# Kernel optimization log

Hardware: AMD Instinct MI355X
Metric: run time of the kernel (lower is better)

Reference implementation:

```python
import jax, jax.numpy as jnp
import numpy as np

N_NODES = 100000

def graph_conv(x, src, dst, W_rel, W_root, b, num_nodes):
    # PyG GraphConv: out_i = lin_rel(sum_{j in N(i)} x_j) + lin_root(x_i)
    agg = jax.ops.segment_sum(x[src], dst, num_segments=num_nodes)  # [N, F_in]
    return agg @ W_rel + x @ W_root + b


def setup_inputs() -> dict:
    key = jax.random.key(0)
    ks = jax.random.split(key, 8)
    z = jax.random.normal(ks[0], (N_NODES, 64), dtype=jnp.float32)
    edge_index = jax.random.randint(ks[1], (2, 1600000), 0, N_NODES, dtype=jnp.int64)
    def glorot(k, fi, fo):
        s = (6.0 / (fi + fo)) ** 0.5
        return jax.random.uniform(k, (fi, fo), dtype=jnp.float32, minval=-s, maxval=s)
    return {
        "z": z,
        "edge_index": edge_index,
        "W_rel1": glorot(ks[2], 64, 32), "W_root1": glorot(ks[3], 64, 32), "b1": jnp.zeros((32,), jnp.float32),
        "W_rel2": glorot(ks[4], 32, 16), "W_root2": glorot(ks[5], 32, 16), "b2": jnp.zeros((16,), jnp.float32),
        "W_rel3": glorot(ks[6], 16, 2), "W_root3": glorot(ks[7], 16, 2), "b3": jnp.zeros((2,), jnp.float32),
    }


def reference(z, edge_index, W_rel1, W_root1, b1, W_rel2, W_root2, b2, W_rel3, W_root3, b3):
    src, dst = edge_index[0], edge_index[1]
    h = graph_conv(z, src, dst, W_rel1, W_root1, b1, N_NODES)
    h = jax.nn.relu(h)
    h = graph_conv(h, src, dst, W_rel2, W_root2, b2, N_NODES)
    h = jax.nn.relu(h)
    h = graph_conv(h, src, dst, W_rel3, W_root3, b3, N_NODES)
    return jax.nn.softmax(h, axis=-1)
```

## Files before the change

kernel.cpp:

```cpp
#include <hip/hip_runtime.h>


#define RNODES 128
#define NB_MAX 1024
#define CH 4096
#define CMAX 512

template <int Fin, int Fout, bool RELU>
__global__ void linear_q2_kernel(const float* __restrict__ x,
                                 const float* __restrict__ Wrel,
                                 const float* __restrict__ Wroot,
                                 const float* __restrict__ bias,
                                 short* __restrict__ t,
                                 float* __restrict__ tscale,
                                 float* __restrict__ acc, int N) {
    const bool rootTask = (blockIdx.y != 0);
    const float* __restrict__ W = rootTask ? Wroot : Wrel;

    int n = blockIdx.x * blockDim.x + threadIdx.x;
    if (n >= N) return;

    float o[Fout];
#pragma unroll
    for (int f = 0; f < Fout; ++f) o[f] = 0.f;

    const float* xr = x + (size_t)n * Fin;
#pragma unroll
    for (int k = 0; k < Fin; k += 4) {
        float4 v = *(const float4*)(xr + k);
        if (RELU) {
            v.x = fmaxf(v.x, 0.f); v.y = fmaxf(v.y, 0.f);
            v.z = fmaxf(v.z, 0.f); v.w = fmaxf(v.w, 0.f);
        }
        const float xv[4] = {v.x, v.y, v.z, v.w};
#pragma unroll
        for (int kk = 0; kk < 4; ++kk) {
            const float* wr = W + (size_t)(k + kk) * Fout;
#pragma unroll
            for (int f = 0; f < Fout; ++f)
                o[f] = fmaf(xv[kk], wr[f], o[f]);
        }
    }

    if (rootTask) {
#pragma unroll
        for (int f = 0; f < Fout; ++f) o[f] += bias[f];
        float* arow = acc + (size_t)n * Fout;
        if constexpr (Fout >= 4) {
#pragma unroll
            for (int f = 0; f < Fout; f += 4)
                *(float4*)(arow + f) = make_float4(o[f], o[f+1], o[f+2], o[f+3]);
        } else {
            *(float2*)arow = make_float2(o[0], o[1]);
        }
    } else {
        float m = 0.f;
#pragma unroll
        for (int f = 0; f < Fout; ++f) m = fmaxf(m, fabsf(o[f]));
        const float inv = (m > 0.f) ? (32767.0f / m) : 0.f;
        const float sc  = m * (1.0f / 32767.0f);

        short q[Fout];
#pragma unroll
        for (int f = 0; f < Fout; ++f) q[f] = (short)__float2int_rn(o[f] * inv);

        if constexpr (Fout == 32) {
            tscale[n] = sc;
            short* trow = t + (size_t)n * 32;
#pragma unroll
            for (int f = 0; f < 32; f += 8)
                *(int4*)(trow + f) = *(const int4*)(q + f);
        } else if constexpr (Fout == 16) {
            short* trow = t + (size_t)n * 32;
            *(int4*)(trow)     = *(const int4*)(q);
            *(int4*)(trow + 8) = *(const int4*)(q + 8);
            ((float*)trow)[8]  = sc;
        } else {
            int2 r;
            r.x = (int)(unsigned short)q[0] | ((int)q[1] << 16);
            r.y = __float_as_int(sc);
            *(int2*)(t + (size_t)n * 4) = r;
        }
    }
}

template <int Fin, int Fout, bool RELU>
__global__ void linear2_kernel(const float* __restrict__ x,
                               const float* __restrict__ Wrel,
                               const float* __restrict__ Wroot,
                               const float* __restrict__ bias,
                               float* __restrict__ t,
                               float* __restrict__ acc, int N) {
    const bool rootTask = (blockIdx.y != 0);
    const float* __restrict__ W = rootTask ? Wroot : Wrel;
    float* __restrict__ outp    = rootTask ? acc : t;

    int n = blockIdx.x * blockDim.x + threadIdx.x;
    if (n >= N) return;

    float o[Fout];
#pragma unroll
    for (int f = 0; f < Fout; ++f) o[f] = 0.f;

    const float* xr = x + (size_t)n * Fin;
#pragma unroll
    for (int k = 0; k < Fin; k += 4) {
        float4 v = *(const float4*)(xr + k);
        if (RELU) {
            v.x = fmaxf(v.x, 0.f); v.y = fmaxf(v.y, 0.f);
            v.z = fmaxf(v.z, 0.f); v.w = fmaxf(v.w, 0.f);
        }
        const float xv[4] = {v.x, v.y, v.z, v.w};
#pragma unroll
        for (int kk = 0; kk < 4; ++kk) {
            const float* wr = W + (size_t)(k + kk) * Fout;
#pragma unroll
            for (int f = 0; f < Fout; ++f)
                o[f] = fmaf(xv[kk], wr[f], o[f]);
        }
    }
    if (rootTask) {
#pragma unroll
        for (int f = 0; f < Fout; ++f) o[f] += bias[f];
    }
    float* op = outp + (size_t)n * Fout;
    if constexpr (Fout >= 4) {
#pragma unroll
        for (int f = 0; f < Fout; f += 4)
            *(float4*)(op + f) = make_float4(o[f], o[f + 1], o[f + 2], o[f + 3]);
    } else {
        *(float2*)op = make_float2(o[0], o[1]);
    }
}

__global__ void hist_chunked_kernel(const int* __restrict__ dst,
                                    int* __restrict__ chunkhist,
                                    int nE, int NB) {
    __shared__ int h[NB_MAX];
    const int c  = blockIdx.x;
    const int e0 = c * CH, e1 = min(e0 + CH, nE);
    for (int b = threadIdx.x; b < NB; b += blockDim.x) h[b] = 0;
    __syncthreads();
    for (int e = e0 + threadIdx.x; e < e1; e += blockDim.x)
        atomicAdd(&h[dst[e] >> 7], 1);
    __syncthreads();
    for (int b = threadIdx.x; b < NB; b += blockDim.x)
        chunkhist[(size_t)c * NB + b] = h[b];
}

__global__ void scan_chunkhist_kernel(int* __restrict__ chunkhist,
                                      int* __restrict__ gtotal,
                                      int C, int NB) {
    __shared__ int s[CMAX];
    const int b = blockIdx.x;
    const int t = threadIdx.x;
    int v = (t < C) ? chunkhist[(size_t)t * NB + b] : 0;
    s[t] = v;
    __syncthreads();
    for (int off = 1; off < CMAX; off <<= 1) {
        int u = (t >= off) ? s[t - off] : 0;
        __syncthreads();
        s[t] += u;
        __syncthreads();
    }
    if (t < C) chunkhist[(size_t)t * NB + b] = s[t] - v;
    if (t == CMAX - 1) gtotal[b] = s[t];
}

__global__ void scan_buckets_kernel(const int* __restrict__ gtotal,
                                    int* __restrict__ bptr, int NB, int nE) {
    __shared__ int s[NB_MAX];
    int t = threadIdx.x;
    int own = (t < NB) ? gtotal[t] : 0;
    s[t] = own;
    __syncthreads();
    for (int off = 1; off < NB_MAX; off <<= 1) {
        int v = (t >= off) ? s[t - off] : 0;
        __syncthreads();
        s[t] += v;
        __syncthreads();
    }
    if (t < NB) bptr[t] = s[t] - own;
    if (t == 0) bptr[NB] = nE;
}

__global__ void bucketize_det_kernel(const int* __restrict__ src,
                                     const int* __restrict__ dst,
                                     const int* __restrict__ chunkpre,
                                     const int* __restrict__ bptr,
                                     unsigned int* __restrict__ records,
                                     int nE, int NB) {
    __shared__ int lcur[NB_MAX];
    const int c  = blockIdx.x;
    const int e0 = c * CH, e1 = min(e0 + CH, nE);
    for (int b = threadIdx.x; b < NB; b += blockDim.x)
        lcur[b] = bptr[b] + chunkpre[(size_t)c * NB + b];
    __syncthreads();
    for (int e = e0 + threadIdx.x; e < e1; e += blockDim.x) {
        int d = dst[e];
        int b = d >> 7;
        int pos = atomicAdd(&lcur[b], 1);
        records[pos] = (unsigned int)src[e] | ((unsigned int)(d & 127) << 17);
    }
}

__global__ void place_merge_kernel(const unsigned int* __restrict__ records,
                                   const int* __restrict__ bptr,
                                   int* __restrict__ rowptr,
                                   int* __restrict__ srcs_sorted,
                                   int N, int nE, int NB) {
    __shared__ int hist[RNODES];
    __shared__ int s[RNODES];
    __shared__ int lcur[RNODES];
    const int b    = blockIdx.x;
    const int base = b * RNODES;
    const int nn   = min(RNODES, N - base);
    const int beg  = bptr[b], end = bptr[b + 1];
    const int t    = threadIdx.x;

    if (t < RNODES) hist[t] = 0;
    __syncthreads();
    for (int i = beg + t; i < end; i += blockDim.x)
        atomicAdd(&hist[records[i] >> 17], 1);
    __syncthreads();

    if (t < RNODES) s[t] = hist[t];
    __syncthreads();
    for (int off = 1; off < RNODES; off <<= 1) {
        int v = (t < RNODES && t >= off) ? s[t - off] : 0;
        __syncthreads();
        if (t < RNODES && t >= off) s[t] += v;
        __syncthreads();
    }
    if (t < nn) {
        int ex = beg + s[t] - hist[t];
        rowptr[base + t] = ex;
        lcur[t] = ex;
    }
    if (b == NB - 1 && t == 0) rowptr[N] = nE;
    __syncthreads();

    for (int i = beg + t; i < end; i += blockDim.x) {
        unsigned int rec = records[i];
        int pos = atomicAdd(&lcur[rec >> 17], 1);
        srcs_sorted[pos] = (int)(rec & 0x1FFFFu);
    }
}

template <int F, bool SOFTMAX>
__global__ void gather_agg_q_kernel(const short* __restrict__ t,
                                    const float* __restrict__ tscale,
                                    const int* __restrict__ rowptr,
                                    const int* __restrict__ srcs,
                                    const float* __restrict__ rootacc,
                                    float* __restrict__ out, int N) {
    constexpr int P = (F >= 4) ? (F / 2) : 1;
    constexpr int S = F / 2;
    int tid = blockIdx.x * blockDim.x + threadIdx.x;
    int n  = (P == 1) ? tid : (tid / P);
    int fp = (P == 1) ? 0   : (tid & (P - 1));
    if (n >= N) return;

    const int* tp = (const int*)t;
    int beg = rowptr[n], end = rowptr[n + 1];
    float sx = 0.f, sy = 0.f;
    int e = beg;
    for (; e + 8 <= end; e += 8) {
        int s[8];
#pragma unroll
        for (int u = 0; u < 8; ++u) s[u] = srcs[e + u];
        int q[8]; float sc[8];
#pragma unroll
        for (int u = 0; u < 8; ++u) {
            q[u]  = tp[s[u] * S + fp];
            sc[u] = tscale[s[u]];
        }
#pragma unroll
        for (int u = 0; u < 8; ++u) {
            float lo = (float)((short)(q[u] & 0xFFFF));
            float hi = (float)(q[u] >> 16);
            sx = fmaf(sc[u], lo, sx);
            sy = fmaf(sc[u], hi, sy);
        }
    }
    for (; e < end; ++e) {
        int s0 = srcs[e];
        int qv = tp[s0 * S + fp];
        float sc = tscale[s0];
        sx = fmaf(sc, (float)((short)(qv & 0xFFFF)), sx);
        sy = fmaf(sc, (float)(qv >> 16), sy);
    }

    const float2 r0 = *(const float2*)(rootacc + (size_t)n * F + 2 * fp);
    float a = r0.x + sx, b = r0.y + sy;
    if (!SOFTMAX) {
        *(float2*)(out + (size_t)n * F + 2 * fp) = make_float2(a, b);
    } else {
        float m = fmaxf(a, b);
        float ea = __expf(a - m), eb = __expf(b - m);
        float inv = 1.0f / (ea + eb);
        *(float2*)(out + (size_t)n * 2) = make_float2(ea * inv, eb * inv);
    }
}

__global__ void gather16_inl_kernel(const short* __restrict__ t,
                                    const int* __restrict__ rowptr,
                                    const int* __restrict__ srcs,
                                    const float* __restrict__ rootacc,
                                    float* __restrict__ out, int N) {
    int tid = blockIdx.x * blockDim.x + threadIdx.x;
    int n  = tid >> 3;
    int fp = tid & 7;
    if (n >= N) return;

    const int* tp = (const int*)t;
    int beg = rowptr[n], end = rowptr[n + 1];
    float sx = 0.f, sy = 0.f;
    int e = beg;
    for (; e + 8 <= end; e += 8) {
        int s[8];
#pragma unroll
        for (int u = 0; u < 8; ++u) s[u] = srcs[e + u];
        int q[8]; float sc[8];
#pragma unroll
        for (int u = 0; u < 8; ++u) {
            const int* row = tp + (size_t)s[u] * 16;
            q[u]  = row[fp];
            sc[u] = __int_as_float(row[8]);
        }
#pragma unroll
        for (int u = 0; u < 8; ++u) {
            sx = fmaf(sc[u], (float)((short)(q[u] & 0xFFFF)), sx);
            sy = fmaf(sc[u], (float)(q[u] >> 16), sy);
        }
    }
    for (; e < end; ++e) {
        const int* row = tp + (size_t)srcs[e] * 16;
        int qv = row[fp];
        float sc = __int_as_float(row[8]);
        sx = fmaf(sc, (float)((short)(qv & 0xFFFF)), sx);
        sy = fmaf(sc, (float)(qv >> 16), sy);
    }

    const float2 r0 = *(const float2*)(rootacc + (size_t)n * 16 + 2 * fp);
    *(float2*)(out + (size_t)n * 16 + 2 * fp) = make_float2(r0.x + sx, r0.y + sy);
}

__global__ void gather2_inl_kernel(const short* __restrict__ t,
                                   const int* __restrict__ rowptr,
                                   const int* __restrict__ srcs,
                                   const float* __restrict__ rootacc,
                                   float* __restrict__ out, int N) {
    int tid = blockIdx.x * blockDim.x + threadIdx.x;
    int n  = tid >> 2;
    int fp = tid & 3;
    if (n >= N) return;

    const int2* tp = (const int2*)t;
    int beg = rowptr[n], end = rowptr[n + 1];
    float sx = 0.f, sy = 0.f;
    int e = beg + fp;
    for (; e + 12 < end; e += 16) {
        int s0 = srcs[e], s1 = srcs[e + 4], s2 = srcs[e + 8], s3 = srcs[e + 12];
        int2 r0 = tp[s0], r1 = tp[s1], r2 = tp[s2], r3 = tp[s3];
        sx = fmaf(__int_as_float(r0.y), (float)((short)(r0.x & 0xFFFF)), sx);
        sy = fmaf(__int_as_float(r0.y), (float)(r0.x >> 16), sy);
        sx = fmaf(__int_as_float(r1.y), (float)((short)(r1.x & 0xFFFF)), sx);
        sy = fmaf(__int_as_float(r1.y), (float)(r1.x >> 16), sy);
        sx = fmaf(__int_as_float(r2.y), (float)((short)(r2.x & 0xFFFF)), sx);
        sy = fmaf(__int_as_float(r2.y), (float)(r2.x >> 16), sy);
        sx = fmaf(__int_as_float(r3.y), (float)((short)(r3.x & 0xFFFF)), sx);
        sy = fmaf(__int_as_float(r3.y), (float)(r3.x >> 16), sy);
    }
    for (; e < end; e += 4) {
        int2 r = tp[srcs[e]];
        sx = fmaf(__int_as_float(r.y), (float)((short)(r.x & 0xFFFF)), sx);
        sy = fmaf(__int_as_float(r.y), (float)(r.x >> 16), sy);
    }
    sx += __shfl_xor(sx, 1, 64); sy += __shfl_xor(sy, 1, 64);
    sx += __shfl_xor(sx, 2, 64); sy += __shfl_xor(sy, 2, 64);

    if (fp == 0) {
        const float2 r0 = *(const float2*)(rootacc + (size_t)n * 2);
        float a = r0.x + sx, b = r0.y + sy;
        float m = fmaxf(a, b);
        float ea = __expf(a - m), eb = __expf(b - m);
        float inv = 1.0f / (ea + eb);
        *(float2*)(out + (size_t)n * 2) = make_float2(ea * inv, eb * inv);
    }
}

template <int F>
__global__ void scatter_kernel(const float* __restrict__ t,
                               const int* __restrict__ src,
                               const int* __restrict__ dst,
                               float* __restrict__ acc, int nE) {
    int tid = blockIdx.x * blockDim.x + threadIdx.x;
    int e = tid / F;
    if (e >= nE) return;
    int f = tid & (F - 1);
    atomicAdd(acc + (long)dst[e] * F + f, t[(long)src[e] * F + f]);
}

__global__ void softmax2_kernel(const float* __restrict__ h, float* __restrict__ out, int N) {
    int n = blockIdx.x * blockDim.x + threadIdx.x;
    if (n >= N) return;
    float a = h[2 * n], b = h[2 * n + 1];
    float m = fmaxf(a, b);
    float ea = __expf(a - m), eb = __expf(b - m);
    float inv = 1.0f / (ea + eb);
    out[2 * n] = ea * inv;
    out[2 * n + 1] = eb * inv;
}

extern "C" void kernel_launch(void* const* d_in, const int* in_sizes, int n_in,
                              void* d_out, int out_size, void* d_ws, size_t ws_size,
                              hipStream_t stream) {
    const float* z      = (const float*)d_in[0];
    const int*   ei     = (const int*)d_in[1];
    const float* Wrel1  = (const float*)d_in[2];
    const float* Wroot1 = (const float*)d_in[3];
    const float* b1     = (const float*)d_in[4];
    const float* Wrel2  = (const float*)d_in[5];
    const float* Wroot2 = (const float*)d_in[6];
    const float* b2     = (const float*)d_in[7];
    const float* Wrel3  = (const float*)d_in[8];
    const float* Wroot3 = (const float*)d_in[9];
    const float* b3     = (const float*)d_in[10];

    const int N  = in_sizes[0] / 64;
    const int nE = in_sizes[1] / 2;
    const int* src = ei;
    const int* dst = ei + nE;
    const int NB = (N + RNODES - 1) / RNODES;
    const int C  = (nE + CH - 1) / CH;

    char* wsb = (char*)d_ws;
    size_t off = 0;
    auto take = [&](size_t bytes) -> void* {
        void* p = (void*)(wsb + off);
        off = (off + bytes + 255) & ~(size_t)255;
        return p;
    };
    int*          chunkhist   = (int*)take((size_t)CMAX * NB_MAX * 4);
    int*          gtotal      = (int*)take((size_t)NB_MAX * 4);
    int*          bptr        = (int*)take((size_t)(NB_MAX + 1) * 4);
    unsigned int* records     = (unsigned int*)take((size_t)nE * 4);
    int*          rowptr      = (int*)take((size_t)(N + 1) * 4);
    int*          srcs_sorted = (int*)take((size_t)nE * 4);
    short*        t1          = (short*)take((size_t)N * 32 * 2);
    float*        s1          = (float*)take((size_t)N * 4);
    float*        h1          = (float*)take((size_t)N * 32 * 4);
    short*        t2          = (short*)take((size_t)N * 64);
    float*        h2          = (float*)take((size_t)N * 16 * 4);
    short*        t3          = (short*)take((size_t)N * 8);
    float*        h3          = (float*)take((size_t)N * 2 * 4);
    const size_t needed = off;

    const int B = 256;
    const int nodeBlocks = (N + B - 1) / B;
    const dim3 linGrid(nodeBlocks, 2);
    const bool packOK = (N <= (1 << 17)) && (NB <= NB_MAX) && (C <= CMAX);

    if (ws_size >= needed && packOK) {
        hist_chunked_kernel<<<C, 512, 0, stream>>>(dst, chunkhist, nE, NB);
        scan_chunkhist_kernel<<<NB, CMAX, 0, stream>>>(chunkhist, gtotal, C, NB);
        scan_buckets_kernel<<<1, NB_MAX, 0, stream>>>(gtotal, bptr, NB, nE);
        bucketize_det_kernel<<<C, 512, 0, stream>>>(src, dst, chunkhist, bptr, records, nE, NB);
        place_merge_kernel<<<NB, 512, 0, stream>>>(records, bptr, rowptr, srcs_sorted, N, nE, NB);

        linear_q2_kernel<64, 32, false><<<linGrid, B, 0, stream>>>(
            z, Wrel1, Wroot1, b1, t1, s1, h1, N);
        gather_agg_q_kernel<32, false><<<((size_t)N * 16 + B - 1) / B, B, 0, stream>>>(
            t1, s1, rowptr, srcs_sorted, h1, h1, N);

        linear_q2_kernel<32, 16, true><<<linGrid, B, 0, stream>>>(
            h1, Wrel2, Wroot2, b2, t2, nullptr, h2, N);
        gather16_inl_kernel<<<((size_t)N * 8 + B - 1) / B, B, 0, stream>>>(
            t2, rowptr, srcs_sorted, h2, h2, N);

        linear_q2_kernel<16, 2, true><<<linGrid, B, 0, stream>>>(
            h2, Wrel3, Wroot3, b3, t3, nullptr, h3, N);
        gather2_inl_kernel<<<((size_t)N * 4 + B - 1) / B, B, 0, stream>>>(
            t3, rowptr, srcs_sorted, h3, (float*)d_out, N);
    } else {
        float* regionA = (float*)d_ws;
        float* regionB = regionA + (size_t)N * 32;
        float* ft1 = regionA;
        float* fh1 = regionB;
        float* ft2 = regionA;
        float* fh2 = regionA + (size_t)N * 16;
        float* ft3 = regionB;
        float* fh3 = regionB + (size_t)N * 2;
        linear2_kernel<64, 32, false><<<linGrid, B, 0, stream>>>(z, Wrel1, Wroot1, b1, ft1, fh1, N);
        scatter_kernel<32><<<((size_t)nE * 32 + B - 1) / B, B, 0, stream>>>(ft1, src, dst, fh1, nE);
        linear2_kernel<32, 16, true><<<linGrid, B, 0, stream>>>(fh1, Wrel2, Wroot2, b2, ft2, fh2, N);
        scatter_kernel<16><<<((size_t)nE * 16 + B - 1) / B, B, 0, stream>>>(ft2, src, dst, fh2, nE);
        linear2_kernel<16, 2, true><<<linGrid, B, 0, stream>>>(fh2, Wrel3, Wroot3, b3, ft3, fh3, N);
        scatter_kernel<2><<<((size_t)nE * 2 + B - 1) / B, B, 0, stream>>>(ft3, src, dst, fh3, nE);
        softmax2_kernel<<<nodeBlocks, B, 0, stream>>>(fh3, (float*)d_out, N);
    }
}
```

Measured before the change: 243.0 us.

## Fuse layer-1 linear into sort kernels and drop bucket-scan launch

The layer-1 rel and root linear passes are folded into the histogram and chunk-scan kernels as extra grid rows (blockIdx.y). This lets the dense compute share launches with, and overlap, the latency-bound sort stages. The standalone bucket-scan kernel is removed: bucketize recomputes the bucket prefix in shared memory in every block, and place_merge reduces gtotal per block to find its range. This cuts two launches and one dependency step, at the cost of redundant per-block scans and reductions and larger 1024-thread blocks.

```diff
diff --git a/kernel.cpp b/kernel.cpp
--- a/kernel.cpp
+++ b/kernel.cpp
@@ -5,6 +5,79 @@
 #define NB_MAX 1024
 #define CH 4096
 #define CMAX 512
+
+template <int Fin, int Fout, bool RELU>
+__device__ __forceinline__ void lin_compute(const float* __restrict__ x,
+                                            const float* __restrict__ W,
+                                            int n, float* o) {
+#pragma unroll
+    for (int f = 0; f < Fout; ++f) o[f] = 0.f;
+    const float* xr = x + (size_t)n * Fin;
+#pragma unroll
+    for (int k = 0; k < Fin; k += 4) {
+        float4 v = *(const float4*)(xr + k);
+        if (RELU) {
+            v.x = fmaxf(v.x, 0.f); v.y = fmaxf(v.y, 0.f);
+            v.z = fmaxf(v.z, 0.f); v.w = fmaxf(v.w, 0.f);
+        }
+        const float xv[4] = {v.x, v.y, v.z, v.w};
+#pragma unroll
+        for (int kk = 0; kk < 4; ++kk) {
+            const float* wr = W + (size_t)(k + kk) * Fout;
+#pragma unroll
+            for (int f = 0; f < Fout; ++f)
+                o[f] = fmaf(xv[kk], wr[f], o[f]);
+        }
+    }
+}
+
+template <int Fout>
+__device__ __forceinline__ void store_quant(short* __restrict__ t,
+                                            float* __restrict__ tscale,
+                                            int n, const float* o) {
+    float m = 0.f;
+#pragma unroll
+    for (int f = 0; f < Fout; ++f) m = fmaxf(m, fabsf(o[f]));
+    const float inv = (m > 0.f) ? (32767.0f / m) : 0.f;
+    const float sc  = m * (1.0f / 32767.0f);
+    short q[Fout];
+#pragma unroll
+    for (int f = 0; f < Fout; ++f) q[f] = (short)__float2int_rn(o[f] * inv);
+
+    if constexpr (Fout == 32) {
+        tscale[n] = sc;
+        short* trow = t + (size_t)n * 32;
+#pragma unroll
+        for (int f = 0; f < 32; f += 8)
+            *(int4*)(trow + f) = *(const int4*)(q + f);
+    } else if constexpr (Fout == 16) {
+        short* trow = t + (size_t)n * 32;
+        *(int4*)(trow)     = *(const int4*)(q);
+        *(int4*)(trow + 8) = *(const int4*)(q + 8);
+        ((float*)trow)[8]  = sc;
+    } else {
+        int2 r;
+        r.x = (int)(unsigned short)q[0] | ((int)q[1] << 16);
+        r.y = __float_as_int(sc);
+        *(int2*)(t + (size_t)n * 4) = r;
+    }
+}
+
+template <int Fout>
+__device__ __forceinline__ void store_root(float* __restrict__ acc,
+                                           const float* __restrict__ bias,
+                                           int n, float* o) {
+#pragma unroll
+    for (int f = 0; f < Fout; ++f) o[f] += bias[f];
+    float* arow = acc + (size_t)n * Fout;
+    if constexpr (Fout >= 4) {
+#pragma unroll
+        for (int f = 0; f < Fout; f += 4)
+            *(float4*)(arow + f) = make_float4(o[f], o[f+1], o[f+2], o[f+3]);
+    } else {
+        *(float2*)arow = make_float2(o[0], o[1]);
+    }
+}
 
 template <int Fin, int Fout, bool RELU>
 __global__ void linear_q2_kernel(const float* __restrict__ x,
@@ -14,163 +87,85 @@
                                  short* __restrict__ t,
                                  float* __restrict__ tscale,
                                  float* __restrict__ acc, int N) {
-    const bool rootTask = (blockIdx.y != 0);
-    const float* __restrict__ W = rootTask ? Wroot : Wrel;
-
     int n = blockIdx.x * blockDim.x + threadIdx.x;
     if (n >= N) return;
-
     float o[Fout];
-#pragma unroll
-    for (int f = 0; f < Fout; ++f) o[f] = 0.f;
-
-    const float* xr = x + (size_t)n * Fin;
-#pragma unroll
-    for (int k = 0; k < Fin; k += 4) {
-        float4 v = *(const float4*)(xr + k);
-        if (RELU) {
-            v.x = fmaxf(v.x, 0.f); v.y = fmaxf(v.y, 0.f);
-            v.z = fmaxf(v.z, 0.f); v.w = fmaxf(v.w, 0.f);
-        }
-        const float xv[4] = {v.x, v.y, v.z, v.w};
-#pragma unroll
-        for (int kk = 0; kk < 4; ++kk) {
-            const float* wr = W + (size_t)(k + kk) * Fout;
-#pragma unroll
-            for (int f = 0; f < Fout; ++f)
-                o[f] = fmaf(xv[kk], wr[f], o[f]);
-        }
-    }
-
-    if (rootTask) {
-#pragma unroll
-        for (int f = 0; f < Fout; ++f) o[f] += bias[f];
-        float* arow = acc + (size_t)n * Fout;
-        if constexpr (Fout >= 4) {
-#pragma unroll
-            for (int f = 0; f < Fout; f += 4)
-                *(float4*)(arow + f) = make_float4(o[f], o[f+1], o[f+2], o[f+3]);
-        } else {
-            *(float2*)arow = make_float2(o[0], o[1]);
-        }
-    } else {
-        float m = 0.f;
-#pragma unroll
-        for (int f = 0; f < Fout; ++f) m = fmaxf(m, fabsf(o[f]));
-        const float inv = (m > 0.f) ? (32767.0f / m) : 0.f;
-        const float sc  = m * (1.0f / 32767.0f);
-
-        short q[Fout];
-#pragma unroll
-        for (int f = 0; f < Fout; ++f) q[f] = (short)__float2int_rn(o[f] * inv);
-
-        if constexpr (Fout == 32) {
-            tscale[n] = sc;
-            short* trow = t + (size_t)n * 32;
-#pragma unroll
-            for (int f = 0; f < 32; f += 8)
-                *(int4*)(trow + f) = *(const int4*)(q + f);
-        } else if constexpr (Fout == 16) {
-            short* trow = t + (size_t)n * 32;
-            *(int4*)(trow)     = *(const int4*)(q);
-            *(int4*)(trow + 8) = *(const int4*)(q + 8);
-            ((float*)trow)[8]  = sc;
-        } else {
-            int2 r;
-            r.x = (int)(unsigned short)q[0] | ((int)q[1] << 16);
-            r.y = __float_as_int(sc);
-            *(int2*)(t + (size_t)n * 4) = r;
-        }
-    }
-}
-
-template <int Fin, int Fout, bool RELU>
-__global__ void linear2_kernel(const float* __restrict__ x,
-                               const float* __restrict__ Wrel,
-                               const float* __restrict__ Wroot,
-                               const float* __restrict__ bias,
-                               float* __restrict__ t,
-                               float* __restrict__ acc, int N) {
-    const bool rootTask = (blockIdx.y != 0);
-    const float* __restrict__ W = rootTask ? Wroot : Wrel;
-    float* __restrict__ outp    = rootTask ? acc : t;
-
-    int n = blockIdx.x * blockDim.x + threadIdx.x;
-    if (n >= N) return;
-
-    float o[Fout];
-#pragma unroll
-    for (int f = 0; f < Fout; ++f) o[f] = 0.f;
-
-    const float* xr = x + (size_t)n * Fin;
-#pragma unroll
-    for (int k = 0; k < Fin; k += 4) {
-        float4 v = *(const float4*)(xr + k);
-        if (RELU) {
-            v.x = fmaxf(v.x, 0.f); v.y = fmaxf(v.y, 0.f);
-            v.z = fmaxf(v.z, 0.f); v.w = fmaxf(v.w, 0.f);
-        }
-        const float xv[4] = {v.x, v.y, v.z, v.w};
-#pragma unroll
-        for (int kk = 0; kk < 4; ++kk) {
-            const float* wr = W + (size_t)(k + kk) * Fout;
-#pragma unroll
-            for (int f = 0; f < Fout; ++f)
-                o[f] = fmaf(xv[kk], wr[f], o[f]);
-        }
-    }
-    if (rootTask) {
-#pragma unroll
-        for (int f = 0; f < Fout; ++f) o[f] += bias[f];
-    }
-    float* op = outp + (size_t)n * Fout;
-    if constexpr (Fout >= 4) {
-#pragma unroll
-        for (int f = 0; f < Fout; f += 4)
-            *(float4*)(op + f) = make_float4(o[f], o[f + 1], o[f + 2], o[f + 3]);
-    } else {
-        *(float2*)op = make_float2(o[0], o[1]);
-    }
-}
-
-__global__ void hist_chunked_kernel(const int* __restrict__ dst,
-                                    int* __restrict__ chunkhist,
+    if (blockIdx.y != 0) {
+        lin_compute<Fin, Fout, RELU>(x, Wroot, n, o);
+        store_root<Fout>(acc, bias, n, o);
+    } else {
+        lin_compute<Fin, Fout, RELU>(x, Wrel, n, o);
+        store_quant<Fout>(t, tscale, n, o);
+    }
+}
+
+__global__ void k1_hist_lin1rel_kernel(const int* __restrict__ dst,
+                                       int* __restrict__ chunkhist,
+                                       int nE, int NB,
+                                       const float* __restrict__ z,
+                                       const float* __restrict__ Wrel1,
+                                       short* __restrict__ t1,
+                                       float* __restrict__ s1, int N) {
+    if (blockIdx.y == 0) {
+        __shared__ int h[NB_MAX];
+        const int c  = blockIdx.x;
+        const int e0 = c * CH, e1 = min(e0 + CH, nE);
+        for (int b = threadIdx.x; b < NB; b += blockDim.x) h[b] = 0;
+        __syncthreads();
+        for (int e = e0 + threadIdx.x; e < e1; e += blockDim.x)
+            atomicAdd(&h[dst[e] >> 7], 1);
+        __syncthreads();
+        for (int b = threadIdx.x; b < NB; b += blockDim.x)
+            chunkhist[(size_t)c * NB + b] = h[b];
+    } else {
+        int n = blockIdx.x * blockDim.x + threadIdx.x;
+        if (n >= N) return;
+        float o[32];
+        lin_compute<64, 32, false>(z, Wrel1, n, o);
+        store_quant<32>(t1, s1, n, o);
+    }
+}
+
+__global__ void k2_scan_lin1root_kernel(int* __restrict__ chunkhist,
+                                        int* __restrict__ gtotal,
+                                        int C, int NB,
+                                        const float* __restrict__ z,
+                                        const float* __restrict__ Wroot1,
+                                        const float* __restrict__ b1,
+                                        float* __restrict__ h1, int N) {
+    if (blockIdx.y == 0) {
+        __shared__ int s[CMAX];
+        const int b = blockIdx.x;
+        const int t = threadIdx.x;
+        int v = (t < C) ? chunkhist[(size_t)t * NB + b] : 0;
+        s[t] = v;
+        __syncthreads();
+        for (int off = 1; off < CMAX; off <<= 1) {
+            int u = (t >= off) ? s[t - off] : 0;
+            __syncthreads();
+            s[t] += u;
+            __syncthreads();
+        }
+        if (t < C) chunkhist[(size_t)t * NB + b] = s[t] - v;
+        if (t == CMAX - 1) gtotal[b] = s[t];
+    } else {
+        int n = blockIdx.x * blockDim.x + threadIdx.x;
+        if (n >= N) return;
+        float o[32];
+        lin_compute<64, 32, false>(z, Wroot1, n, o);
+        store_root<32>(h1, b1, n, o);
+    }
+}
+
+__global__ void k3_bucketize_kernel(const int* __restrict__ src,
+                                    const int* __restrict__ dst,
+                                    const int* __restrict__ chunkpre,
+                                    const int* __restrict__ gtotal,
+                                    unsigned int* __restrict__ records,
                                     int nE, int NB) {
-    __shared__ int h[NB_MAX];
-    const int c  = blockIdx.x;
-    const int e0 = c * CH, e1 = min(e0 + CH, nE);
-    for (int b = threadIdx.x; b < NB; b += blockDim.x) h[b] = 0;
-    __syncthreads();
-    for (int e = e0 + threadIdx.x; e < e1; e += blockDim.x)
-        atomicAdd(&h[dst[e] >> 7], 1);
-    __syncthreads();
-    for (int b = threadIdx.x; b < NB; b += blockDim.x)
-        chunkhist[(size_t)c * NB + b] = h[b];
-}
-
-__global__ void scan_chunkhist_kernel(int* __restrict__ chunkhist,
-                                      int* __restrict__ gtotal,
-                                      int C, int NB) {
-    __shared__ int s[CMAX];
-    const int b = blockIdx.x;
+    __shared__ int s[NB_MAX];
+    __shared__ int lcur[NB_MAX];
     const int t = threadIdx.x;
-    int v = (t < C) ? chunkhist[(size_t)t * NB + b] : 0;
-    s[t] = v;
-    __syncthreads();
-    for (int off = 1; off < CMAX; off <<= 1) {
-        int u = (t >= off) ? s[t - off] : 0;
-        __syncthreads();
-        s[t] += u;
-        __syncthreads();
-    }
-    if (t < C) chunkhist[(size_t)t * NB + b] = s[t] - v;
-    if (t == CMAX - 1) gtotal[b] = s[t];
-}
-
-__global__ void scan_buckets_kernel(const int* __restrict__ gtotal,
-                                    int* __restrict__ bptr, int NB, int nE) {
-    __shared__ int s[NB_MAX];
-    int t = threadIdx.x;
     int own = (t < NB) ? gtotal[t] : 0;
     s[t] = own;
     __syncthreads();
@@ -180,23 +175,12 @@
         s[t] += v;
         __syncthreads();
     }
-    if (t < NB) bptr[t] = s[t] - own;
-    if (t == 0) bptr[NB] = nE;
-}
-
-__global__ void bucketize_det_kernel(const int* __restrict__ src,
-                                     const int* __restrict__ dst,
-                                     const int* __restrict__ chunkpre,
-                                     const int* __restrict__ bptr,
-                                     unsigned int* __restrict__ records,
-                                     int nE, int NB) {
-    __shared__ int lcur[NB_MAX];
-    const int c  = blockIdx.x;
+    const int c = blockIdx.x;
+    for (int b = t; b < NB; b += blockDim.x)
+        lcur[b] = (s[b] - gtotal[b]) + chunkpre[(size_t)c * NB + b];
+    __syncthreads();
     const int e0 = c * CH, e1 = min(e0 + CH, nE);
-    for (int b = threadIdx.x; b < NB; b += blockDim.x)
-        lcur[b] = bptr[b] + chunkpre[(size_t)c * NB + b];
-    __syncthreads();
-    for (int e = e0 + threadIdx.x; e < e1; e += blockDim.x) {
+    for (int e = e0 + t; e < e1; e += blockDim.x) {
         int d = dst[e];
         int b = d >> 7;
         int pos = atomicAdd(&lcur[b], 1);
@@ -204,19 +188,29 @@
     }
 }
 
-__global__ void place_merge_kernel(const unsigned int* __restrict__ records,
-                                   const int* __restrict__ bptr,
-                                   int* __restrict__ rowptr,
-                                   int* __restrict__ srcs_sorted,
-                                   int N, int nE, int NB) {
+__global__ void k4_place_merge_kernel(const unsigned int* __restrict__ records,
+                                      const int* __restrict__ gtotal,
+                                      int* __restrict__ rowptr,
+                                      int* __restrict__ srcs_sorted,
+                                      int N, int nE, int NB) {
+    __shared__ int red[NB_MAX];
     __shared__ int hist[RNODES];
     __shared__ int s[RNODES];
     __shared__ int lcur[RNODES];
-    const int b    = blockIdx.x;
+    const int b = blockIdx.x;
+    const int t = threadIdx.x;
+
+    red[t] = (t < b) ? gtotal[t] : 0;
+    __syncthreads();
+    for (int off = NB_MAX / 2; off > 0; off >>= 1) {
+        if (t < off) red[t] += red[t + off];
+        __syncthreads();
+    }
+    const int beg = red[0];
+    const int end = beg + gtotal[b];
+
     const int base = b * RNODES;
     const int nn   = min(RNODES, N - base);
-    const int beg  = bptr[b], end = bptr[b + 1];
-    const int t    = threadIdx.x;
 
     if (t < RNODES) hist[t] = 0;
     __syncthreads();
@@ -390,6 +384,36 @@
     }
 }
 
+template <int Fin, int Fout, bool RELU>
+__global__ void linear2_kernel(const float* __restrict__ x,
+                               const float* __restrict__ Wrel,
+                               const float* __restrict__ Wroot,
+                               const float* __restrict__ bias,
+                               float* __restrict__ t,
+                               float* __restrict__ acc, int N) {
+    const bool rootTask = (blockIdx.y != 0);
+    const float* __restrict__ W = rootTask ? Wroot : Wrel;
+    float* __restrict__ outp    = rootTask ? acc : t;
+
+    int n = blockIdx.x * blockDim.x + threadIdx.x;
+    if (n >= N) return;
+
+    float o[Fout];
+    lin_compute<Fin, Fout, RELU>(x, W, n, o);
+    if (rootTask) {
+#pragma unroll
+        for (int f = 0; f < Fout; ++f) o[f] += bias[f];
+    }
+    float* op = outp + (size_t)n * Fout;
+    if constexpr (Fout >= 4) {
+#pragma unroll
+        for (int f = 0; f < Fout; f += 4)
+            *(float4*)(op + f) = make_float4(o[f], o[f + 1], o[f + 2], o[f + 3]);
+    } else {
+        *(float2*)op = make_float2(o[0], o[1]);
+    }
+}
+
 template <int F>
 __global__ void scatter_kernel(const float* __restrict__ t,
                                const int* __restrict__ src,
@@ -444,7 +468,6 @@
     };
     int*          chunkhist   = (int*)take((size_t)CMAX * NB_MAX * 4);
     int*          gtotal      = (int*)take((size_t)NB_MAX * 4);
-    int*          bptr        = (int*)take((size_t)(NB_MAX + 1) * 4);
     unsigned int* records     = (unsigned int*)take((size_t)nE * 4);
     int*          rowptr      = (int*)take((size_t)(N + 1) * 4);
     int*          srcs_sorted = (int*)take((size_t)nE * 4);
@@ -463,14 +486,15 @@
     const bool packOK = (N <= (1 << 17)) && (NB <= NB_MAX) && (C <= CMAX);
 
     if (ws_size >= needed && packOK) {
-        hist_chunked_kernel<<<C, 512, 0, stream>>>(dst, chunkhist, nE, NB);
-        scan_chunkhist_kernel<<<NB, CMAX, 0, stream>>>(chunkhist, gtotal, C, NB);
-        scan_buckets_kernel<<<1, NB_MAX, 0, stream>>>(gtotal, bptr, NB, nE);
-        bucketize_det_kernel<<<C, 512, 0, stream>>>(src, dst, chunkhist, bptr, records, nE, NB);
-        place_merge_kernel<<<NB, 512, 0, stream>>>(records, bptr, rowptr, srcs_sorted, N, nE, NB);
-
-        linear_q2_kernel<64, 32, false><<<linGrid, B, 0, stream>>>(
-            z, Wrel1, Wroot1, b1, t1, s1, h1, N);
+        k1_hist_lin1rel_kernel<<<dim3(C, 2), 512, 0, stream>>>(
+            dst, chunkhist, nE, NB, z, Wrel1, t1, s1, N);
+        k2_scan_lin1root_kernel<<<dim3(NB, 2), CMAX, 0, stream>>>(
+            chunkhist, gtotal, C, NB, z, Wroot1, b1, h1, N);
+        k3_bucketize_kernel<<<C, NB_MAX, 0, stream>>>(
+            src, dst, chunkhist, gtotal, records, nE, NB);
+        k4_place_merge_kernel<<<NB, NB_MAX, 0, stream>>>(
+            records, gtotal, rowptr, srcs_sorted, N, nE, NB);
+
         gather_agg_q_kernel<32, false><<<((size_t)N * 16 + B - 1) / B, B, 0, stream>>>(
             t1, s1, rowptr, srcs_sorted, h1, h1, N);
 
```

After: 255.7 us. 5.2% more time.

## Share int16 quantization scale per 128-node group instead of per node

Applied to the files above, without the earlier changes.

Replaces the per-node quantization scale with one scale per group of 128 nodes, computed by a wave shuffle max plus a shared-memory combine in the linear kernel. The quantized rows shrink: layer 2 drops from 64 to 32 bytes and layer 3 from 8 to 4 bytes, and the per-edge scale lookups go to a small table that should stay cached. This is meant to cut gather traffic in the three aggregation kernels. In exchange, precision drops for nodes whose magnitude is much smaller than the group maximum, and the linear kernel gains a block barrier.

```diff
diff --git a/kernel.cpp b/kernel.cpp
--- a/kernel.cpp
+++ b/kernel.cpp
@@ -7,23 +7,11 @@
 #define CMAX 512
 
 template <int Fin, int Fout, bool RELU>
-__global__ void linear_q2_kernel(const float* __restrict__ x,
-                                 const float* __restrict__ Wrel,
-                                 const float* __restrict__ Wroot,
-                                 const float* __restrict__ bias,
-                                 short* __restrict__ t,
-                                 float* __restrict__ tscale,
-                                 float* __restrict__ acc, int N) {
-    const bool rootTask = (blockIdx.y != 0);
-    const float* __restrict__ W = rootTask ? Wroot : Wrel;
-
-    int n = blockIdx.x * blockDim.x + threadIdx.x;
-    if (n >= N) return;
-
-    float o[Fout];
+__device__ __forceinline__ void lin_compute(const float* __restrict__ x,
+                                            const float* __restrict__ W,
+                                            int n, float* o) {
 #pragma unroll
     for (int f = 0; f < Fout; ++f) o[f] = 0.f;
-
     const float* xr = x + (size_t)n * Fin;
 #pragma unroll
     for (int k = 0; k < Fin; k += 4) {
@@ -41,8 +29,23 @@
                 o[f] = fmaf(xv[kk], wr[f], o[f]);
         }
     }
-
-    if (rootTask) {
+}
+
+template <int Fin, int Fout, bool RELU>
+__global__ void linear_qg_kernel(const float* __restrict__ x,
+                                 const float* __restrict__ Wrel,
+                                 const float* __restrict__ Wroot,
+                                 const float* __restrict__ bias,
+                                 short* __restrict__ t,
+                                 float* __restrict__ gscale,
+                                 float* __restrict__ acc, int N) {
+    int n = blockIdx.x * blockDim.x + threadIdx.x;
+    const bool valid = (n < N);
+    float o[Fout];
+
+    if (blockIdx.y != 0) {
+        if (!valid) return;
+        lin_compute<Fin, Fout, RELU>(x, Wroot, n, o);
 #pragma unroll
         for (int f = 0; f < Fout; ++f) o[f] += bias[f];
         float* arow = acc + (size_t)n * Fout;
@@ -53,83 +56,43 @@
         } else {
             *(float2*)arow = make_float2(o[0], o[1]);
         }
+        return;
+    }
+
+    float m = 0.f;
+    if (valid) {
+        lin_compute<Fin, Fout, RELU>(x, Wrel, n, o);
+#pragma unroll
+        for (int f = 0; f < Fout; ++f) m = fmaxf(m, fabsf(o[f]));
+    }
+    float wm = m;
+#pragma unroll
+    for (int off = 1; off < 64; off <<= 1)
+        wm = fmaxf(wm, __shfl_xor(wm, off, 64));
+    __shared__ float wmax[4];
+    const int wv = threadIdx.x >> 6;
+    if ((threadIdx.x & 63) == 0) wmax[wv] = wm;
+    __syncthreads();
+    const float g = fmaxf(wmax[wv & 2], wmax[(wv & 2) | 1]);
+    if (!valid) return;
+    const float inv = (g > 0.f) ? (32767.0f / g) : 0.f;
+    if ((threadIdx.x & 127) == 0) gscale[n >> 7] = g * (1.0f / 32767.0f);
+
+    short q[Fout];
+#pragma unroll
+    for (int f = 0; f < Fout; ++f) q[f] = (short)__float2int_rn(o[f] * inv);
+
+    if constexpr (Fout == 32) {
+        short* trow = t + (size_t)n * 32;
+#pragma unroll
+        for (int f = 0; f < 32; f += 8)
+            *(int4*)(trow + f) = *(const int4*)(q + f);
+    } else if constexpr (Fout == 16) {
+        short* trow = t + (size_t)n * 16;
+        *(int4*)(trow)     = *(const int4*)(q);
+        *(int4*)(trow + 8) = *(const int4*)(q + 8);
     } else {
-        float m = 0.f;
-#pragma unroll
-        for (int f = 0; f < Fout; ++f) m = fmaxf(m, fabsf(o[f]));
-        const float inv = (m > 0.f) ? (32767.0f / m) : 0.f;
-        const float sc  = m * (1.0f / 32767.0f);
-
-        short q[Fout];
-#pragma unroll
-        for (int f = 0; f < Fout; ++f) q[f] = (short)__float2int_rn(o[f] * inv);
-
-        if constexpr (Fout == 32) {
-            tscale[n] = sc;
-            short* trow = t + (size_t)n * 32;
-#pragma unroll
-            for (int f = 0; f < 32; f += 8)
-                *(int4*)(trow + f) = *(const int4*)(q + f);
-        } else if constexpr (Fout == 16) {
-            short* trow = t + (size_t)n * 32;
-            *(int4*)(trow)     = *(const int4*)(q);
-            *(int4*)(trow + 8) = *(const int4*)(q + 8);
-            ((float*)trow)[8]  = sc;
-        } else {
-            int2 r;
-            r.x = (int)(unsigned short)q[0] | ((int)q[1] << 16);
-            r.y = __float_as_int(sc);
-            *(int2*)(t + (size_t)n * 4) = r;
-        }
-    }
-}
-
-template <int Fin, int Fout, bool RELU>
-__global__ void linear2_kernel(const float* __restrict__ x,
-                               const float* __restrict__ Wrel,
-                               const float* __restrict__ Wroot,
-                               const float* __restrict__ bias,
-                               float* __restrict__ t,
-                               float* __restrict__ acc, int N) {
-    const bool rootTask = (blockIdx.y != 0);
-    const float* __restrict__ W = rootTask ? Wroot : Wrel;
-    float* __restrict__ outp    = rootTask ? acc : t;
-
-    int n = blockIdx.x * blockDim.x + threadIdx.x;
-    if (n >= N) return;
-
-    float o[Fout];
-#pragma unroll
-    for (int f = 0; f < Fout; ++f) o[f] = 0.f;
-
-    const float* xr = x + (size_t)n * Fin;
-#pragma unroll
-    for (int k = 0; k < Fin; k += 4) {
-        float4 v = *(const float4*)(xr + k);
-        if (RELU) {
-            v.x = fmaxf(v.x, 0.f); v.y = fmaxf(v.y, 0.f);
-            v.z = fmaxf(v.z, 0.f); v.w = fmaxf(v.w, 0.f);
-        }
-        const float xv[4] = {v.x, v.y, v.z, v.w};
-#pragma unroll
-        for (int kk = 0; kk < 4; ++kk) {
-            const float* wr = W + (size_t)(k + kk) * Fout;
-#pragma unroll
-            for (int f = 0; f < Fout; ++f)
-                o[f] = fmaf(xv[kk], wr[f], o[f]);
-        }
-    }
-    if (rootTask) {
-#pragma unroll
-        for (int f = 0; f < Fout; ++f) o[f] += bias[f];
-    }
-    float* op = outp + (size_t)n * Fout;
-    if constexpr (Fout >= 4) {
-#pragma unroll
-        for (int f = 0; f < Fout; f += 4)
-            *(float4*)(op + f) = make_float4(o[f], o[f + 1], o[f + 2], o[f + 3]);
-    } else {
-        *(float2*)op = make_float2(o[0], o[1]);
+        ((int*)t)[n] = (int)(unsigned short)q[0] | ((int)q[1] << 16);
     }
 }
 
@@ -247,18 +210,15 @@
     }
 }
 
-template <int F, bool SOFTMAX>
-__global__ void gather_agg_q_kernel(const short* __restrict__ t,
-                                    const float* __restrict__ tscale,
-                                    const int* __restrict__ rowptr,
-                                    const int* __restrict__ srcs,
-                                    const float* __restrict__ rootacc,
-                                    float* __restrict__ out, int N) {
-    constexpr int P = (F >= 4) ? (F / 2) : 1;
-    constexpr int S = F / 2;
+__global__ void gather32_g_kernel(const short* __restrict__ t,
+                                  const float* __restrict__ gscale,
+                                  const int* __restrict__ rowptr,
+                                  const int* __restrict__ srcs,
+                                  const float* __restrict__ rootacc,
+                                  float* __restrict__ out, int N) {
     int tid = blockIdx.x * blockDim.x + threadIdx.x;
-    int n  = (P == 1) ? tid : (tid / P);
-    int fp = (P == 1) ? 0   : (tid & (P - 1));
+    int n  = tid >> 4;
+    int fp = tid & 15;
     if (n >= N) return;
 
     const int* tp = (const int*)t;
@@ -272,42 +232,33 @@
         int q[8]; float sc[8];
 #pragma unroll
         for (int u = 0; u < 8; ++u) {
-            q[u]  = tp[s[u] * S + fp];
-            sc[u] = tscale[s[u]];
+            q[u]  = tp[(size_t)s[u] * 16 + fp];
+            sc[u] = gscale[s[u] >> 7];
         }
 #pragma unroll
         for (int u = 0; u < 8; ++u) {
-            float lo = (float)((short)(q[u] & 0xFFFF));
-            float hi = (float)(q[u] >> 16);
-            sx = fmaf(sc[u], lo, sx);
-            sy = fmaf(sc[u], hi, sy);
+            sx = fmaf(sc[u], (float)((short)(q[u] & 0xFFFF)), sx);
+            sy = fmaf(sc[u], (float)(q[u] >> 16), sy);
         }
     }
     for (; e < end; ++e) {
         int s0 = srcs[e];
-        int qv = tp[s0 * S + fp];
-        float sc = tscale[s0];
+        int qv = tp[(size_t)s0 * 16 + fp];
+        float sc = gscale[s0 >> 7];
         sx = fmaf(sc, (float)((short)(qv & 0xFFFF)), sx);
         sy = fmaf(sc, (float)(qv >> 16), sy);
     }
 
-    const float2 r0 = *(const float2*)(rootacc + (size_t)n * F + 2 * fp);
-    float a = r0.x + sx, b = r0.y + sy;
-    if (!SOFTMAX) {
-        *(float2*)(out + (size_t)n * F + 2 * fp) = make_float2(a, b);
-    } else {
-        float m = fmaxf(a, b);
-        float ea = __expf(a - m), eb = __expf(b - m);
-        float inv = 1.0f / (ea + eb);
-        *(float2*)(out + (size_t)n * 2) = make_float2(ea * inv, eb * inv);
-    }
-}
-
-__global__ void gather16_inl_kernel(const short* __restrict__ t,
-                                    const int* __restrict__ rowptr,
-                                    const int* __restrict__ srcs,
-                                    const float* __restrict__ rootacc,
-                                    float* __restrict__ out, int N) {
+    const float2 r0 = *(const float2*)(rootacc + (size_t)n * 32 + 2 * fp);
+    *(float2*)(out + (size_t)n * 32 + 2 * fp) = make_float2(r0.x + sx, r0.y + sy);
+}
+
+__global__ void gather16_g_kernel(const short* __restrict__ t,
+                                  const float* __restrict__ gscale,
+                                  const int* __restrict__ rowptr,
+                                  const int* __restrict__ srcs,
+                                  const float* __restrict__ rootacc,
+                                  float* __restrict__ out, int N) {
     int tid = blockIdx.x * blockDim.x + threadIdx.x;
     int n  = tid >> 3;
     int fp = tid & 7;
@@ -324,9 +275,8 @@
         int q[8]; float sc[8];
 #pragma unroll
         for (int u = 0; u < 8; ++u) {
-            const int* row = tp + (size_t)s[u] * 16;
-            q[u]  = row[fp];
-            sc[u] = __int_as_float(row[8]);
+            q[u]  = tp[(size_t)s[u] * 8 + fp];
+            sc[u] = gscale[s[u] >> 7];
         }
 #pragma unroll
         for (int u = 0; u < 8; ++u) {
@@ -335,9 +285,9 @@
         }
     }
     for (; e < end; ++e) {
-        const int* row = tp + (size_t)srcs[e] * 16;
-        int qv = row[fp];
-        float sc = __int_as_float(row[8]);
+        int s0 = srcs[e];
+        int qv = tp[(size_t)s0 * 8 + fp];
+        float sc = gscale[s0 >> 7];
         sx = fmaf(sc, (float)((short)(qv & 0xFFFF)), sx);
         sy = fmaf(sc, (float)(qv >> 16), sy);
     }
@@ -346,36 +296,41 @@
     *(float2*)(out + (size_t)n * 16 + 2 * fp) = make_float2(r0.x + sx, r0.y + sy);
 }
 
-__global__ void gather2_inl_kernel(const short* __restrict__ t,
-                                   const int* __restrict__ rowptr,
-                                   const int* __restrict__ srcs,
-                                   const float* __restrict__ rootacc,
-                                   float* __restrict__ out, int N) {
+__global__ void gather2_g_kernel(const short* __restrict__ t,
+                                 const float* __restrict__ gscale,
+                                 const int* __restrict__ rowptr,
+                                 const int* __restrict__ srcs,
+                                 const float* __restrict__ rootacc,
+                                 float* __restrict__ out, int N) {
     int tid = blockIdx.x * blockDim.x + threadIdx.x;
     int n  = tid >> 2;
     int fp = tid & 3;
     if (n >= N) return;
 
-    const int2* tp = (const int2*)t;
+    const int* tp = (const int*)t;
     int beg = rowptr[n], end = rowptr[n + 1];
     float sx = 0.f, sy = 0.f;
     int e = beg + fp;
     for (; e + 12 < end; e += 16) {
         int s0 = srcs[e], s1 = srcs[e + 4], s2 = srcs[e + 8], s3 = srcs[e + 12];
-        int2 r0 = tp[s0], r1 = tp[s1], r2 = tp[s2], r3 = tp[s3];
-        sx = fmaf(__int_as_float(r0.y), (float)((short)(r0.x & 0xFFFF)), sx);
-        sy = fmaf(__int_as_float(r0.y), (float)(r0.x >> 16), sy);
-        sx = fmaf(__int_as_float(r1.y), (float)((short)(r1.x & 0xFFFF)), sx);
-        sy = fmaf(__int_as_float(r1.y), (float)(r1.x >> 16), sy);
-        sx = fmaf(__int_as_float(r2.y), (float)((short)(r2.x & 0xFFFF)), sx);
-        sy = fmaf(__int_as_float(r2.y), (float)(r2.x >> 16), sy);
-        sx = fmaf(__int_as_float(r3.y), (float)((short)(r3.x & 0xFFFF)), sx);
-        sy = fmaf(__int_as_float(r3.y), (float)(r3.x >> 16), sy);
+        int r0 = tp[s0], r1 = tp[s1], r2 = tp[s2], r3 = tp[s3];
+        float c0 = gscale[s0 >> 7], c1 = gscale[s1 >> 7];
+        float c2 = gscale[s2 >> 7], c3 = gscale[s3 >> 7];
+        sx = fmaf(c0, (float)((short)(r0 & 0xFFFF)), sx);
+        sy = fmaf(c0, (float)(r0 >> 16), sy);
+        sx = fmaf(c1, (float)((short)(r1 & 0xFFFF)), sx);
+        sy = fmaf(c1, (float)(r1 >> 16), sy);
+        sx = fmaf(c2, (float)((short)(r2 & 0xFFFF)), sx);
+        sy = fmaf(c2, (float)(r2 >> 16), sy);
+        sx = fmaf(c3, (float)((short)(r3 & 0xFFFF)), sx);
+        sy = fmaf(c3, (float)(r3 >> 16), sy);
     }
     for (; e < end; e += 4) {
-        int2 r = tp[srcs[e]];
-        sx = fmaf(__int_as_float(r.y), (float)((short)(r.x & 0xFFFF)), sx);
-        sy = fmaf(__int_as_float(r.y), (float)(r.x >> 16), sy);
+        int s0 = srcs[e];
+        int r = tp[s0];
+        float c = gscale[s0 >> 7];
+        sx = fmaf(c, (float)((short)(r & 0xFFFF)), sx);
+        sy = fmaf(c, (float)(r >> 16), sy);
     }
     sx += __shfl_xor(sx, 1, 64); sy += __shfl_xor(sy, 1, 64);
     sx += __shfl_xor(sx, 2, 64); sy += __shfl_xor(sy, 2, 64);
@@ -387,6 +342,36 @@
         float ea = __expf(a - m), eb = __expf(b - m);
         float inv = 1.0f / (ea + eb);
         *(float2*)(out + (size_t)n * 2) = make_float2(ea * inv, eb * inv);
+    }
+}
+
+template <int Fin, int Fout, bool RELU>
+__global__ void linear2_kernel(const float* __restrict__ x,
+                               const float* __restrict__ Wrel,
+                               const float* __restrict__ Wroot,
+                               const float* __restrict__ bias,
+                               float* __restrict__ t,
+                               float* __restrict__ acc, int N) {
+    const bool rootTask = (blockIdx.y != 0);
+    const float* __restrict__ W = rootTask ? Wroot : Wrel;
+    float* __restrict__ outp    = rootTask ? acc : t;
+
+    int n = blockIdx.x * blockDim.x + threadIdx.x;
+    if (n >= N) return;
+
+    float o[Fout];
+    lin_compute<Fin, Fout, RELU>(x, W, n, o);
+    if (rootTask) {
+#pragma unroll
+        for (int f = 0; f < Fout; ++f) o[f] += bias[f];
+    }
+    float* op = outp + (size_t)n * Fout;
+    if constexpr (Fout >= 4) {
+#pragma unroll
+        for (int f = 0; f < Fout; f += 4)
+            *(float4*)(op + f) = make_float4(o[f], o[f + 1], o[f + 2], o[f + 3]);
+    } else {
+        *(float2*)op = make_float2(o[0], o[1]);
     }
 }
 
@@ -449,11 +434,13 @@
     int*          rowptr      = (int*)take((size_t)(N + 1) * 4);
     int*          srcs_sorted = (int*)take((size_t)nE * 4);
     short*        t1          = (short*)take((size_t)N * 32 * 2);
-    float*        s1          = (float*)take((size_t)N * 4);
+    float*        gs1         = (float*)take((size_t)NB_MAX * 4);
     float*        h1          = (float*)take((size_t)N * 32 * 4);
-    short*        t2          = (short*)take((size_t)N * 64);
+    short*        t2          = (short*)take((size_t)N * 16 * 2);
+    float*        gs2         = (float*)take((size_t)NB_MAX * 4);
     float*        h2          = (float*)take((size_t)N * 16 * 4);
-    short*        t3          = (short*)take((size_t)N * 8);
+    short*        t3          = (short*)take((size_t)N * 2 * 2);
+    float*        gs3         = (float*)take((size_t)NB_MAX * 4);
     float*        h3          = (float*)take((size_t)N * 2 * 4);
     const size_t needed = off;
 
@@ -469,20 +456,20 @@
         bucketize_det_kernel<<<C, 512, 0, stream>>>(src, dst, chunkhist, bptr, records, nE, NB);
         place_merge_kernel<<<NB, 512, 0, stream>>>(records, bptr, rowptr, srcs_sorted, N, nE, NB);
 
-        linear_q2_kernel<64, 32, false><<<linGrid, B, 0, stream>>>(
-            z, Wrel1, Wroot1, b1, t1, s1, h1, N);
-        gather_agg_q_kernel<32, false><<<((size_t)N * 16 + B - 1) / B, B, 0, stream>>>(
-            t1, s1, rowptr, srcs_sorted, h1, h1, N);
-
-        linear_q2_kernel<32, 16, true><<<linGrid, B, 0, stream>>>(
-            h1, Wrel2, Wroot2, b2, t2, nullptr, h2, N);
-        gather16_inl_kernel<<<((size_t)N * 8 + B - 1) / B, B, 0, stream>>>(
-            t2, rowptr, srcs_sorted, h2, h2, N);
-
-        linear_q2_kernel<16, 2, true><<<linGrid, B, 0, stream>>>(
-            h2, Wrel3, Wroot3, b3, t3, nullptr, h3, N);
-        gather2_inl_kernel<<<((size_t)N * 4 + B - 1) / B, B, 0, stream>>>(
-            t3, rowptr, srcs_sorted, h3, (float*)d_out, N);
+        linear_qg_kernel<64, 32, false><<<linGrid, B, 0, stream>>>(
+            z, Wrel1, Wroot1, b1, t1, gs1, h1, N);
+        gather32_g_kernel<<<((size_t)N * 16 + B - 1) / B, B, 0, stream>>>(
+            t1, gs1, rowptr, srcs_sorted, h1, h1, N);
+
+        linear_qg_kernel<32, 16, true><<<linGrid, B, 0, stream>>>(
+            h1, Wrel2, Wroot2, b2, t2, gs2, h2, N);
+        gather16_g_kernel<<<((size_t)N * 8 + B - 1) / B, B, 0, stream>>>(
+            t2, gs2, rowptr, srcs_sorted, h2, h2, N);
+
+        linear_qg_kernel<16, 2, true><<<linGrid, B, 0, stream>>>(
+            h2, Wrel3, Wroot3, b3, t3, gs3, h3, N);
+        gather2_g_kernel<<<((size_t)N * 4 + B - 1) / B, B, 0, stream>>>(
+            t3, gs3, rowptr, srcs_sorted, h3, (float*)d_out, N);
     } else {
         float* regionA = (float*)d_ws;
         float* regionB = regionA + (size_t)N * 32;
```

Measured after the change: 234.7 us. 1.04x faster.
